# Kernel optimization log

Measured on AMD Instinct MI355X. Metric: run time of the kernel, lower is better.

Reference implementation:

```python
import jax, jax.numpy as jnp
import numpy as np

# Static config (matches init_kwargs)
DIM = 1024
INTER = 512
E = 8          # n_routed_experts
TOP_K = 2      # n_activated_experts
ROUTE_SCALE = 1.0


def setup_inputs() -> dict:
    key = jax.random.key(0)
    ks = jax.random.split(key, 8)
    s_d = 1.0 / np.sqrt(DIM)
    s_f = 1.0 / np.sqrt(INTER)
    x = jax.random.normal(ks[0], (2, 2048, DIM), dtype=jnp.float32)
    gate_w = jax.random.uniform(ks[1], (E, DIM), jnp.float32, -s_d, s_d)
    # routed expert weights, stacked: gate/up are [E, F, D], down is [E, D, F]
    wg = jax.random.uniform(ks[2], (E, INTER, DIM), jnp.float32, -s_d, s_d)
    wu = jax.random.uniform(ks[3], (E, INTER, DIM), jnp.float32, -s_d, s_d)
    wd = jax.random.uniform(ks[4], (E, DIM, INTER), jnp.float32, -s_f, s_f)
    # shared expert (n_shared_experts = 1)
    sg = jax.random.uniform(ks[5], (INTER, DIM), jnp.float32, -s_d, s_d)
    su = jax.random.uniform(ks[6], (INTER, DIM), jnp.float32, -s_d, s_d)
    sd = jax.random.uniform(ks[7], (DIM, INTER), jnp.float32, -s_f, s_f)
    return {"x": x, "gate_w": gate_w, "wg": wg, "wu": wu, "wd": wd,
            "sg": sg, "su": su, "sd": sd}


def reference(x, gate_w, wg, wu, wd, sg, su, sd):
    B, S, D = x.shape
    xf = x.reshape(-1, D)                       # [N, D]
    N = xf.shape[0]

    # ---- Gate (eval mode: no expert_bias, softmax scoring, 1 group) ----
    scores = jax.nn.softmax(xf @ gate_w.T, axis=-1)          # [N, E]
    _, idx = jax.lax.top_k(scores, TOP_K)                    # [N, K]
    weights = jnp.take_along_axis(scores, idx, axis=-1) * ROUTE_SCALE  # [N, K]

    # Combine weights as dense [N, E] (scatter-add of top-k weights) --
    # equivalent to the sort/dispatch + weighted scatter_add combine.
    cw = jnp.zeros((N, E), dtype=xf.dtype)
    cw = cw.at[jnp.arange(N)[:, None], idx].add(weights)     # [N, E]

    # ---- Routed experts: SwiGLU per expert ----
    g = jnp.einsum('nd,efd->nef', xf, wg)                    # [N, E, F]
    u = jnp.einsum('nd,efd->nef', xf, wu)                    # [N, E, F]
    h = jax.nn.silu(g) * u                                   # [N, E, F]
    y = jnp.einsum('nef,edf->ned', h, wd)                    # [N, E, D]
    routed = jnp.einsum('ned,ne->nd', y, cw)                 # [N, D]

    # ---- Shared expert (always active) ----
    shared = (jax.nn.silu(xf @ sg.T) * (xf @ su.T)) @ sd.T   # [N, D]

    return (routed + shared).reshape(B, S, D)
```

## Files before the change

kernel.cpp:

```cpp
#include <hip/hip_runtime.h>
#include <hip/hip_bf16.h>

constexpr int NTOK = 4096;
constexpr int DIMD = 1024;
constexpr int FINT = 512;
constexpr int NEXP = 8;

typedef __attribute__((ext_vector_type(8))) short bf16x8;
typedef __attribute__((ext_vector_type(4))) float f32x4;
typedef __attribute__((ext_vector_type(8))) unsigned short u16x8;

__device__ __forceinline__ f32x4 mfma16(bf16x8 a, bf16x8 b, f32x4 c) {
  return __builtin_amdgcn_mfma_f32_16x16x32_bf16(a, b, c, 0, 0, 0);
}

__device__ __forceinline__ void gload16(const void* g, void* l) {
  __builtin_amdgcn_global_load_lds(
      (const __attribute__((address_space(1))) void*)g,
      (__attribute__((address_space(3))) void*)l, 16, 0, 0);
}

__device__ __forceinline__ unsigned short f2bf(float f) {
  unsigned u = __float_as_uint(f);
  u += 0x7fffu + ((u >> 16) & 1u);
  return (unsigned short)(u >> 16);
}

__global__ __launch_bounds__(256) void cast_all(
    const float* __restrict__ x,  const float* __restrict__ wg,
    const float* __restrict__ wu, const float* __restrict__ wd,
    const float* __restrict__ sg, const float* __restrict__ su,
    const float* __restrict__ sd, const float* __restrict__ gw,
    unsigned short* __restrict__ xb,  unsigned short* __restrict__ w1b,
    unsigned short* __restrict__ wdb, unsigned short* __restrict__ s1b,
    unsigned short* __restrict__ sdb,
    int* __restrict__ eid, float2* __restrict__ w12) {
  const int seg = blockIdx.y;

  if (seg == 7) {
    if (blockIdx.x >= NTOK / 4) return;
    const int wid = threadIdx.x >> 6;
    const int lane = threadIdx.x & 63;
    const int n = blockIdx.x * 4 + wid;

    const float4* xr = (const float4*)(x + (size_t)n * DIMD);
    float4 xv[4];
#pragma unroll
    for (int j = 0; j < 4; ++j) xv[j] = xr[lane + 64 * j];

    double acc[NEXP];
#pragma unroll
    for (int e = 0; e < NEXP; ++e) {
      const float4* g = (const float4*)(gw + (size_t)e * DIMD);
      double a = 0.0;
#pragma unroll
      for (int j = 0; j < 4; ++j) {
        float4 gv = g[lane + 64 * j];
        a += (double)xv[j].x * (double)gv.x + (double)xv[j].y * (double)gv.y
           + (double)xv[j].z * (double)gv.z + (double)xv[j].w * (double)gv.w;
      }
      acc[e] = a;
    }
#pragma unroll
    for (int e = 0; e < NEXP; ++e) {
#pragma unroll
      for (int off = 32; off > 0; off >>= 1) acc[e] += __shfl_xor(acc[e], off);
    }

    if (lane == 0) {
      float logit[NEXP];
#pragma unroll
      for (int e = 0; e < NEXP; ++e) logit[e] = (float)acc[e];
      int i1 = 0; float v1 = logit[0];
#pragma unroll
      for (int e = 1; e < NEXP; ++e) if (logit[e] > v1) { v1 = logit[e]; i1 = e; }
      int i2 = -1; float v2 = -1e30f;
#pragma unroll
      for (int e = 0; e < NEXP; ++e) if (e != i1 && logit[e] > v2) { v2 = logit[e]; i2 = e; }
      float s = 0.f;
#pragma unroll
      for (int e = 0; e < NEXP; ++e) s += expf(logit[e] - v1);
      float w1 = 1.f / s;
      float w2 = expf(v2 - v1) / s;
      eid[n] = i1 | (i2 << 4);
      w12[n] = make_float2(w1, w2);
    }
    return;
  }

  const int i = blockIdx.x * 256 + threadIdx.x;
  const float* src; unsigned short* dst;
  size_t si = (size_t)i * 8, di;
  int n8;
  if (seg == 0) {
    n8 = NTOK * DIMD / 8; if (i >= n8) return;
    src = x; dst = xb; di = si;
  } else if (seg == 1 || seg == 2) {
    n8 = NEXP * FINT * DIMD / 8; if (i >= n8) return;
    int e = (int)(si >> 19), f = (int)((si >> 10) & 511), d = (int)(si & 1023);
    int r = ((f >> 4) << 5) + (seg == 2 ? 16 : 0) + (f & 15);
    src = (seg == 1) ? wg : wu; dst = w1b;
    di = (((size_t)e << 10) + r) * 1024 + d;
  } else if (seg == 3) {
    n8 = NEXP * DIMD * FINT / 8; if (i >= n8) return;
    src = wd; dst = wdb; di = si;
  } else if (seg == 4 || seg == 5) {
    n8 = FINT * DIMD / 8; if (i >= n8) return;
    int f = (int)((si >> 10) & 511), d = (int)(si & 1023);
    int r = ((f >> 4) << 5) + (seg == 5 ? 16 : 0) + (f & 15);
    src = (seg == 4) ? sg : su; dst = s1b;
    di = (size_t)r * 1024 + d;
  } else {
    n8 = DIMD * FINT / 8; if (i >= n8) return;
    src = sd; dst = sdb; di = si;
  }
  const float4* s4 = (const float4*)(src + si);
  float4 a = s4[0], b = s4[1];
  u16x8 o;
  o[0] = f2bf(a.x); o[1] = f2bf(a.y); o[2] = f2bf(a.z); o[3] = f2bf(a.w);
  o[4] = f2bf(b.x); o[5] = f2bf(b.y); o[6] = f2bf(b.z); o[7] = f2bf(b.w);
  *(u16x8*)(dst + di) = o;
}

__global__ __launch_bounds__(1024) void dispatch_scan(const int* __restrict__ eid,
                                                      const float2* __restrict__ w12,
                                                      int* __restrict__ cnt,
                                                      int* __restrict__ rowTok,
                                                      float* __restrict__ rowW,
                                                      int2* __restrict__ gslot) {
  const int th = threadIdx.x;
  const int lane = th & 63;
  const int wv = th >> 6;

  int e0[4], e1[4];
  float2 wp[4];
  unsigned long long c0 = 0, c1 = 0;
#pragma unroll
  for (int j = 0; j < 4; ++j) {
    int n = th * 4 + j;
    int p = eid[n];
    wp[j] = w12[n];
    int a = p & 15, b = (p >> 4) & 15;
    e0[j] = a; e1[j] = b;
    unsigned long long ia = 1ull << (16 * (a & 3));
    if (a < 4) c0 += ia; else c1 += ia;
    unsigned long long ib = 1ull << (16 * (b & 3));
    if (b < 4) c0 += ib; else c1 += ib;
  }

  unsigned long long s0 = c0, s1 = c1;
#pragma unroll
  for (int off = 1; off < 64; off <<= 1) {
    unsigned long long u0 = __shfl_up(s0, off);
    unsigned long long u1 = __shfl_up(s1, off);
    if (lane >= off) { s0 += u0; s1 += u1; }
  }

  __shared__ unsigned long long wt0[16], wt1[16];
  __shared__ int ebaseS[NEXP];
  if (lane == 63) { wt0[wv] = s0; wt1[wv] = s1; }
  __syncthreads();

  unsigned long long b0 = 0, b1 = 0;
  for (int w2 = 0; w2 < 16; ++w2)
    if (w2 < wv) { b0 += wt0[w2]; b1 += wt1[w2]; }

  if (th == 0) {
    unsigned long long t0 = 0, t1 = 0;
    for (int w2 = 0; w2 < 16; ++w2) { t0 += wt0[w2]; t1 += wt1[w2]; }
    int tot[NEXP];
#pragma unroll
    for (int e = 0; e < 4; ++e) {
      tot[e]     = (int)((t0 >> (16 * e)) & 0xffff);
      tot[e + 4] = (int)((t1 >> (16 * e)) & 0xffff);
    }
    int run = 0;
#pragma unroll
    for (int e = 0; e < NEXP; ++e) {
      cnt[e] = tot[e];
      cnt[8 + e] = run;
      ebaseS[e] = run;
      run += tot[e];
    }
  }

  unsigned long long x0 = b0 + s0 - c0;
  unsigned long long x1 = b1 + s1 - c1;

  __shared__ unsigned short posL[1024][8];
#pragma unroll
  for (int e = 0; e < 4; ++e) {
    posL[th][e]     = (unsigned short)((x0 >> (16 * e)) & 0xffff);
    posL[th][e + 4] = (unsigned short)((x1 >> (16 * e)) & 0xffff);
  }
  __syncthreads();

#pragma unroll
  for (int j = 0; j < 4; ++j) {
    int n = th * 4 + j;
    int a = e0[j];
    int pa = posL[th][a]; posL[th][a] = (unsigned short)(pa + 1);
    rowTok[a * NTOK + pa] = n; rowW[a * NTOK + pa] = wp[j].x;
    int b = e1[j];
    int pb = posL[th][b]; posL[th][b] = (unsigned short)(pb + 1);
    rowTok[b * NTOK + pb] = n; rowW[b * NTOK + pb] = wp[j].y;
    gslot[n] = make_int2(ebaseS[a] + pa, ebaseS[b] + pb);
  }
}


#define GEMM_TILE_LOOP(NT)                                                     \
  STAGE(0, 0, 0);                                                              \
  STAGE(0, 0, 1);                                                              \
  for (int tt = 0; tt < (NT); ++tt) {                                          \
    const int buf = tt & 1;                                                    \
    const unsigned char* LA0 = L + (buf * 2 + 0) * 16384;                      \
    const unsigned char* LB0 = LA0 + 65536;                                    \
    const unsigned char* LA1 = L + (buf * 2 + 1) * 16384;                      \
    const unsigned char* LB1 = LA1 + 65536;                                    \
    bf16x8 Af[4], Bf[4];                                                       \
                                                            \
    asm volatile("s_waitcnt vmcnt(4)" ::: "memory");                           \
    __builtin_amdgcn_sched_barrier(0);                                         \
    __builtin_amdgcn_s_barrier();                                              \
    __builtin_amdgcn_sched_barrier(0);                                         \
    _Pragma("unroll")                                                          \
    for (int n = 0; n < 4; ++n)                                                \
      Bf[n] = *(const bf16x8*)(LB0 + (wc * 64 + n * 16 + fr) * 64 + koffl);    \
    _Pragma("unroll")                                                          \
    for (int m = 0; m < 4; ++m)                                                \
      Af[m] = *(const bf16x8*)(LA0 + (wr * 128 + m * 16 + fr) * 64 + koffl);   \
    __builtin_amdgcn_s_setprio(1);                                             \
    _Pragma("unroll")                                                          \
    for (int n = 0; n < 4; ++n)                                                \
      _Pragma("unroll")                                                        \
      for (int m = 0; m < 4; ++m)                                              \
        acc[m][n] = mfma16(Af[m], Bf[n], acc[m][n]);                           \
    __builtin_amdgcn_s_setprio(0);                                             \
                                                            \
    if (tt + 1 < (NT)) STAGE(buf ^ 1, tt + 1, 0);                              \
    _Pragma("unroll")                                                          \
    for (int m = 0; m < 4; ++m)                                                \
      Af[m] = *(const bf16x8*)(LA0 + (wr * 128 + (m + 4) * 16 + fr) * 64 + koffl); \
    __builtin_amdgcn_s_setprio(1);                                             \
    _Pragma("unroll")                                                          \
    for (int n = 0; n < 4; ++n)                                                \
      _Pragma("unroll")                                                        \
      for (int m = 0; m < 4; ++m)                                              \
        acc[m + 4][n] = mfma16(Af[m], Bf[n], acc[m + 4][n]);                   \
    __builtin_amdgcn_s_setprio(0);                                             \
                                                            \
    if (tt + 1 < (NT)) asm volatile("s_waitcnt vmcnt(4)" ::: "memory");        \
    else               asm volatile("s_waitcnt vmcnt(0)" ::: "memory");        \
    __builtin_amdgcn_sched_barrier(0);                                         \
    __builtin_amdgcn_s_barrier();                                              \
    __builtin_amdgcn_sched_barrier(0);                                         \
    _Pragma("unroll")                                                          \
    for (int n = 0; n < 4; ++n)                                                \
      Bf[n] = *(const bf16x8*)(LB1 + (wc * 64 + n * 16 + fr) * 64 + koffl);    \
    _Pragma("unroll")                                                          \
    for (int m = 0; m < 4; ++m)                                                \
      Af[m] = *(const bf16x8*)(LA1 + (wr * 128 + m * 16 + fr) * 64 + koffl);   \
    __builtin_amdgcn_s_setprio(1);                                             \
    _Pragma("unroll")                                                          \
    for (int n = 0; n < 4; ++n)                                                \
      _Pragma("unroll")                                                        \
      for (int m = 0; m < 4; ++m)                                              \
        acc[m][n] = mfma16(Af[m], Bf[n], acc[m][n]);                           \
    __builtin_amdgcn_s_setprio(0);                                             \
                                                            \
    if (tt + 1 < (NT)) STAGE(buf ^ 1, tt + 1, 1);                              \
    _Pragma("unroll")                                                          \
    for (int m = 0; m < 4; ++m)                                                \
      Af[m] = *(const bf16x8*)(LA1 + (wr * 128 + (m + 4) * 16 + fr) * 64 + koffl); \
    __builtin_amdgcn_s_setprio(1);                                             \
    _Pragma("unroll")                                                          \
    for (int n = 0; n < 4; ++n)                                                \
      _Pragma("unroll")                                                        \
      for (int m = 0; m < 4; ++m)                                              \
        acc[m + 4][n] = mfma16(Af[m], Bf[n], acc[m + 4][n]);                   \
    __builtin_amdgcn_s_setprio(0);                                             \
  }

__global__ __launch_bounds__(512, 1) void gemm1_fused(
    const unsigned short* __restrict__ xb,
    const unsigned short* __restrict__ w1b,
    const unsigned short* __restrict__ s1b,
    unsigned short* __restrict__ hb,
    unsigned short* __restrict__ hs,
    const int* __restrict__ cnt,
    const int* __restrict__ rowTok,
    const unsigned short* __restrict__ zpg) {
  extern __shared__ unsigned char L[];
  const int e = blockIdx.x >> 2, ty = blockIdx.x & 3;
  const int tx = blockIdx.y;
  const bool RT = (e < NEXP);
  const int Te = RT ? cnt[e] : NTOK;
  const int m0 = tx * 256;
  if (m0 >= Te) return;
  const int n0 = ty * 256;

  const int t = threadIdx.x;
  const int w = t >> 6, lane = t & 63;
  const int wr = w >> 2, wc = w & 3;
  const int fr = lane & 15, hi = lane >> 4;
  const int koffl = ((hi ^ ((fr >> 1) & 3)) << 4);

  const unsigned short* w1e = RT ? w1b + (size_t)e * DIMD * DIMD : s1b;

  const unsigned short* apD[2];
  const unsigned short* bpD[2];
  int aoff[2], boff[2];
#pragma unroll
  for (int j = 0; j < 2; ++j) {
    int c = w * 128 + j * 64 + lane;
    int rowL = c >> 2;
    int seff = (c & 3) ^ ((c >> 3) & 3);
    int grow = m0 + rowL;
    const unsigned short* p;
    if (RT) p = (grow < Te) ? xb + (size_t)rowTok[e * NTOK + grow] * DIMD : zpg;
    else    p = xb + (size_t)grow * DIMD;
    apD[j] = p + seff * 8;
    bpD[j] = w1e + (size_t)(n0 + rowL) * DIMD + seff * 8;
    aoff[j] = c * 16;
    boff[j] = 65536 + c * 16;
  }

  f32x4 acc[8][4];
  f32x4 zero = {0.f, 0.f, 0.f, 0.f};
#pragma unroll
  for (int m = 0; m < 8; ++m)
#pragma unroll
    for (int n = 0; n < 4; ++n) acc[m][n] = zero;

  auto STAGE = [&](int buf, int tt, int q) {
    int slab = (buf * 2 + q) * 16384;
#pragma unroll
    for (int j = 0; j < 2; ++j) {
      gload16(apD[j] + tt * 64 + q * 32, L + slab + aoff[j]);
      gload16(bpD[j] + tt * 64 + q * 32, L + slab + boff[j]);
    }
  };

  GEMM_TILE_LOOP(DIMD / 64)

  unsigned short* hbase = RT ? hb + (size_t)cnt[8 + e] * FINT : hs;
  const int fbase = ty * 128 + wc * 32 + fr;
#pragma unroll
  for (int m = 0; m < 8; ++m) {
#pragma unroll
    for (int r = 0; r < 4; ++r) {
      int row = m0 + wr * 128 + m * 16 + hi * 4 + r;
      if (row < Te) {
        float g0 = acc[m][0][r], u0 = acc[m][1][r];
        float g1 = acc[m][2][r], u1 = acc[m][3][r];
        hbase[(size_t)row * FINT + fbase]      = f2bf(g0 / (1.f + expf(-g0)) * u0);
        hbase[(size_t)row * FINT + fbase + 16] = f2bf(g1 / (1.f + expf(-g1)) * u1);
      }
    }
  }
}

__global__ __launch_bounds__(512, 1) void gemm2_fused(
    const unsigned short* __restrict__ hb,
    const unsigned short* __restrict__ hs,
    const unsigned short* __restrict__ wdb,
    const unsigned short* __restrict__ sdb,
    float* __restrict__ ybuf,
    float* __restrict__ out,
    const int* __restrict__ cnt,
    const float* __restrict__ rowW,
    const unsigned short* __restrict__ zpg) {
  extern __shared__ unsigned char L[];
  const int e = blockIdx.x >> 2, ty = blockIdx.x & 3;
  const int tx = blockIdx.y;
  const bool RT = (e < NEXP);
  const int Te = RT ? cnt[e] : NTOK;
  const int m0 = tx * 256;
  if (m0 >= Te) return;
  const int n0 = ty * 256;

  const int t = threadIdx.x;
  const int w = t >> 6, lane = t & 63;
  const int wr = w >> 2, wc = w & 3;
  const int fr = lane & 15, hi = lane >> 4;
  const int koffl = ((hi ^ ((fr >> 1) & 3)) << 4);

  const int gbase = RT ? cnt[8 + e] : 0;
  const unsigned short* he  = RT ? hb + (size_t)gbase * FINT : hs;
  const unsigned short* wde = RT ? wdb + (size_t)e * DIMD * FINT : sdb;

  const unsigned short* apD[2];
  const unsigned short* bpD[2];
  int aoff[2], boff[2];
#pragma unroll
  for (int j = 0; j < 2; ++j) {
    int c = w * 128 + j * 64 + lane;
    int rowL = c >> 2;
    int seff = (c & 3) ^ ((c >> 3) & 3);
    int grow = m0 + rowL;
    apD[j] = ((grow < Te) ? he + (size_t)grow * FINT : zpg) + seff * 8;
    bpD[j] = wde + (size_t)(n0 + rowL) * FINT + seff * 8;
    aoff[j] = c * 16;
    boff[j] = 65536 + c * 16;
  }

  f32x4 acc[8][4];
  f32x4 zero = {0.f, 0.f, 0.f, 0.f};
#pragma unroll
  for (int m = 0; m < 8; ++m)
#pragma unroll
    for (int n = 0; n < 4; ++n) acc[m][n] = zero;

  auto STAGE = [&](int buf, int tt, int q) {
    int slab = (buf * 2 + q) * 16384;
#pragma unroll
    for (int j = 0; j < 2; ++j) {
      gload16(apD[j] + tt * 64 + q * 32, L + slab + aoff[j]);
      gload16(bpD[j] + tt * 64 + q * 32, L + slab + boff[j]);
    }
  };

  GEMM_TILE_LOOP(FINT / 64)

  const int colb = n0 + wc * 64;
#pragma unroll
  for (int m = 0; m < 8; ++m) {
#pragma unroll
    for (int r = 0; r < 4; ++r) {
      int row = m0 + wr * 128 + m * 16 + hi * 4 + r;
      if (row < Te) {
        if (RT) {
          float wt = rowW[e * NTOK + row];
          float* yr = ybuf + (size_t)(gbase + row) * DIMD;
#pragma unroll
          for (int n = 0; n < 4; ++n)
            yr[colb + n * 16 + fr] = wt * acc[m][n][r];
        } else {
          float* orow = out + (size_t)row * DIMD;
#pragma unroll
          for (int n = 0; n < 4; ++n)
            orow[colb + n * 16 + fr] = acc[m][n][r];
        }
      }
    }
  }
}

__global__ __launch_bounds__(256) void combine(const float* __restrict__ ybuf,
                                               const int2* __restrict__ gslot,
                                               float* __restrict__ out) {
  const int n = blockIdx.x;
  const int t = threadIdx.x;
  int2 gs = gslot[n];
  const float4* y1 = (const float4*)(ybuf + (size_t)gs.x * DIMD);
  const float4* y2 = (const float4*)(ybuf + (size_t)gs.y * DIMD);
  float4* o = (float4*)(out + (size_t)n * DIMD);
  float4 a = o[t], b = y1[t], c = y2[t];
  a.x += b.x + c.x; a.y += b.y + c.y; a.z += b.z + c.z; a.w += b.w + c.w;
  o[t] = a;
}

extern "C" void kernel_launch(void* const* d_in, const int* in_sizes, int n_in,
                              void* d_out, int out_size, void* d_ws, size_t ws_size,
                              hipStream_t stream) {
  const float* x  = (const float*)d_in[0];
  const float* gw = (const float*)d_in[1];
  const float* wg = (const float*)d_in[2];
  const float* wu = (const float*)d_in[3];
  const float* wd = (const float*)d_in[4];
  const float* sg = (const float*)d_in[5];
  const float* su = (const float*)d_in[6];
  const float* sd = (const float*)d_in[7];
  float* out = (float*)d_out;

  char* ws = (char*)d_ws;
  size_t off = 0;
  auto alloc = [&](size_t bytes) -> char* {
    char* p = ws + off;
    off += (bytes + 255) & ~(size_t)255;
    return p;
  };
  unsigned short* xb  = (unsigned short*)alloc((size_t)NTOK * DIMD * 2);
  unsigned short* w1b = (unsigned short*)alloc((size_t)NEXP * DIMD * DIMD * 2);
  unsigned short* wdb = (unsigned short*)alloc((size_t)NEXP * DIMD * FINT * 2);
  unsigned short* s1b = (unsigned short*)alloc((size_t)DIMD * DIMD * 2);
  unsigned short* sdb = (unsigned short*)alloc((size_t)DIMD * FINT * 2);
  unsigned short* hb  = (unsigned short*)alloc((size_t)2 * NTOK * FINT * 2);
  unsigned short* hs  = (unsigned short*)alloc((size_t)NTOK * FINT * 2);
  float*         ybuf = (float*)alloc((size_t)2 * NTOK * DIMD * 4);
  int*            cnt = (int*)alloc(256);
  int*         rowTok = (int*)alloc((size_t)NEXP * NTOK * 4);
  float*         rowW = (float*)alloc((size_t)NEXP * NTOK * 4);
  unsigned short* zpg = (unsigned short*)alloc((size_t)DIMD * 2);
  int*            eid = (int*)alloc((size_t)NTOK * 4);
  float2*         w12 = (float2*)alloc((size_t)NTOK * 8);
  int2*         gslot = (int2*)alloc((size_t)NTOK * 8);
  if (off > ws_size) return;

  hipFuncSetAttribute((const void*)gemm1_fused,
                      hipFuncAttributeMaxDynamicSharedMemorySize, 131072);
  hipFuncSetAttribute((const void*)gemm2_fused,
                      hipFuncAttributeMaxDynamicSharedMemorySize, 131072);

  hipMemsetAsync(zpg, 0, (size_t)DIMD * 2, stream);

  cast_all<<<dim3(2048, 8), 256, 0, stream>>>(x, wg, wu, wd, sg, su, sd, gw,
                                              xb, w1b, wdb, s1b, sdb, eid, w12);

  dispatch_scan<<<1, 1024, 0, stream>>>(eid, w12, cnt, rowTok, rowW, gslot);

  gemm1_fused<<<dim3(36, 16), 512, 131072, stream>>>(xb, w1b, s1b, hb, hs,
                                                     cnt, rowTok, zpg);
  gemm2_fused<<<dim3(36, 16), 512, 131072, stream>>>(hb, hs, wdb, sdb, ybuf, out,
                                                     cnt, rowW, zpg);
  combine<<<NTOK, 256, 0, stream>>>(ybuf, gslot, out);
}
```

Before: 111.9 us.

## Switch GEMMs to 32x32x16 MFMA and store routed outputs in bf16

Result: slower. 122.6 us (+9.5%).

```diff
diff --git a/kernel.cpp b/kernel.cpp
--- a/kernel.cpp
+++ b/kernel.cpp
@@ -7,11 +7,11 @@
 constexpr int NEXP = 8;
 
 typedef __attribute__((ext_vector_type(8))) short bf16x8;
-typedef __attribute__((ext_vector_type(4))) float f32x4;
+typedef __attribute__((ext_vector_type(16))) float f32x16;
 typedef __attribute__((ext_vector_type(8))) unsigned short u16x8;
 
-__device__ __forceinline__ f32x4 mfma16(bf16x8 a, bf16x8 b, f32x4 c) {
-  return __builtin_amdgcn_mfma_f32_16x16x32_bf16(a, b, c, 0, 0, 0);
+__device__ __forceinline__ f32x16 mfma32(bf16x8 a, bf16x8 b, f32x16 c) {
+  return __builtin_amdgcn_mfma_f32_32x32x16_bf16(a, b, c, 0, 0, 0);
 }
 
 __device__ __forceinline__ void gload16(const void* g, void* l) {
@@ -98,7 +98,7 @@
   } else if (seg == 1 || seg == 2) {
     n8 = NEXP * FINT * DIMD / 8; if (i >= n8) return;
     int e = (int)(si >> 19), f = (int)((si >> 10) & 511), d = (int)(si & 1023);
-    int r = ((f >> 4) << 5) + (seg == 2 ? 16 : 0) + (f & 15);
+    int r = ((f >> 5) << 6) + (f & 31) + (seg == 2 ? 32 : 0);
     src = (seg == 1) ? wg : wu; dst = w1b;
     di = (((size_t)e << 10) + r) * 1024 + d;
   } else if (seg == 3) {
@@ -107,7 +107,7 @@
   } else if (seg == 4 || seg == 5) {
     n8 = FINT * DIMD / 8; if (i >= n8) return;
     int f = (int)((si >> 10) & 511), d = (int)(si & 1023);
-    int r = ((f >> 4) << 5) + (seg == 5 ? 16 : 0) + (f & 15);
+    int r = ((f >> 5) << 6) + (f & 31) + (seg == 5 ? 32 : 0);
     src = (seg == 4) ? sg : su; dst = s1b;
     di = (size_t)r * 1024 + d;
   } else {
@@ -209,6 +209,21 @@
 }
 
 
+#define TILE_PHASE(LAx, LBx, KOFF)                                             \
+  _Pragma("unroll")                                                            \
+  for (int m = 0; m < 4; ++m)                                                  \
+    Af[m] = *(const bf16x8*)(LAx + (wr * 128 + m * 32 + l31) * 64 + (KOFF));   \
+  _Pragma("unroll")                                                            \
+  for (int n = 0; n < 2; ++n)                                                  \
+    Bf[n] = *(const bf16x8*)(LBx + (wc * 64 + n * 32 + l31) * 64 + (KOFF));    \
+  __builtin_amdgcn_s_setprio(1);                                               \
+  _Pragma("unroll")                                                            \
+  for (int n = 0; n < 2; ++n)                                                  \
+    _Pragma("unroll")                                                          \
+    for (int m = 0; m < 4; ++m)                                                \
+      acc[m][n] = mfma32(Af[m], Bf[n], acc[m][n]);                             \
+  __builtin_amdgcn_s_setprio(0);
+
 #define GEMM_TILE_LOOP(NT)                                                     \
   STAGE(0, 0, 0);                                                              \
   STAGE(0, 0, 1);                                                              \
@@ -218,68 +233,22 @@
     const unsigned char* LB0 = LA0 + 65536;                                    \
     const unsigned char* LA1 = L + (buf * 2 + 1) * 16384;                      \
     const unsigned char* LB1 = LA1 + 65536;                                    \
-    bf16x8 Af[4], Bf[4];                                                       \
-                                                            \
+    bf16x8 Af[4], Bf[2];                                                       \
     asm volatile("s_waitcnt vmcnt(4)" ::: "memory");                           \
     __builtin_amdgcn_sched_barrier(0);                                         \
     __builtin_amdgcn_s_barrier();                                              \
     __builtin_amdgcn_sched_barrier(0);                                         \
-    _Pragma("unroll")                                                          \
-    for (int n = 0; n < 4; ++n)                                                \
-      Bf[n] = *(const bf16x8*)(LB0 + (wc * 64 + n * 16 + fr) * 64 + koffl);    \
-    _Pragma("unroll")                                                          \
-    for (int m = 0; m < 4; ++m)                                                \
-      Af[m] = *(const bf16x8*)(LA0 + (wr * 128 + m * 16 + fr) * 64 + koffl);   \
-    __builtin_amdgcn_s_setprio(1);                                             \
-    _Pragma("unroll")                                                          \
-    for (int n = 0; n < 4; ++n)                                                \
-      _Pragma("unroll")                                                        \
-      for (int m = 0; m < 4; ++m)                                              \
-        acc[m][n] = mfma16(Af[m], Bf[n], acc[m][n]);                           \
-    __builtin_amdgcn_s_setprio(0);                                             \
-                                                            \
+    TILE_PHASE(LA0, LB0, koff0)                                                \
     if (tt + 1 < (NT)) STAGE(buf ^ 1, tt + 1, 0);                              \
-    _Pragma("unroll")                                                          \
-    for (int m = 0; m < 4; ++m)                                                \
-      Af[m] = *(const bf16x8*)(LA0 + (wr * 128 + (m + 4) * 16 + fr) * 64 + koffl); \
-    __builtin_amdgcn_s_setprio(1);                                             \
-    _Pragma("unroll")                                                          \
-    for (int n = 0; n < 4; ++n)                                                \
-      _Pragma("unroll")                                                        \
-      for (int m = 0; m < 4; ++m)                                              \
-        acc[m + 4][n] = mfma16(Af[m], Bf[n], acc[m + 4][n]);                   \
-    __builtin_amdgcn_s_setprio(0);                                             \
-                                                            \
+    TILE_PHASE(LA0, LB0, koff1)                                                \
     if (tt + 1 < (NT)) asm volatile("s_waitcnt vmcnt(4)" ::: "memory");        \
     else               asm volatile("s_waitcnt vmcnt(0)" ::: "memory");        \
     __builtin_amdgcn_sched_barrier(0);                                         \
     __builtin_amdgcn_s_barrier();                                              \
     __builtin_amdgcn_sched_barrier(0);                                         \
-    _Pragma("unroll")                                                          \
-    for (int n = 0; n < 4; ++n)                                                \
-      Bf[n] = *(const bf16x8*)(LB1 + (wc * 64 + n * 16 + fr) * 64 + koffl);    \
-    _Pragma("unroll")                                                          \
-    for (int m = 0; m < 4; ++m)                                                \
-      Af[m] = *(const bf16x8*)(LA1 + (wr * 128 + m * 16 + fr) * 64 + koffl);   \
-    __builtin_amdgcn_s_setprio(1);                                             \
-    _Pragma("unroll")                                                          \
-    for (int n = 0; n < 4; ++n)                                                \
-      _Pragma("unroll")                                                        \
-      for (int m = 0; m < 4; ++m)                                              \
-        acc[m][n] = mfma16(Af[m], Bf[n], acc[m][n]);                           \
-    __builtin_amdgcn_s_setprio(0);                                             \
-                                                            \
+    TILE_PHASE(LA1, LB1, koff0)                                                \
     if (tt + 1 < (NT)) STAGE(buf ^ 1, tt + 1, 1);                              \
-    _Pragma("unroll")                                                          \
-    for (int m = 0; m < 4; ++m)                                                \
-      Af[m] = *(const bf16x8*)(LA1 + (wr * 128 + (m + 4) * 16 + fr) * 64 + koffl); \
-    __builtin_amdgcn_s_setprio(1);                                             \
-    _Pragma("unroll")                                                          \
-    for (int n = 0; n < 4; ++n)                                                \
-      _Pragma("unroll")                                                        \
-      for (int m = 0; m < 4; ++m)                                              \
-        acc[m + 4][n] = mfma16(Af[m], Bf[n], acc[m + 4][n]);                   \
-    __builtin_amdgcn_s_setprio(0);                                             \
+    TILE_PHASE(LA1, LB1, koff1)                                                \
   }
 
 __global__ __launch_bounds__(512, 1) void gemm1_fused(
@@ -303,8 +272,10 @@
   const int t = threadIdx.x;
   const int w = t >> 6, lane = t & 63;
   const int wr = w >> 2, wc = w & 3;
-  const int fr = lane & 15, hi = lane >> 4;
-  const int koffl = ((hi ^ ((fr >> 1) & 3)) << 4);
+  const int l31 = lane & 31, l5 = lane >> 5;
+  const int sb = (l31 >> 1) & 3;
+  const int koff0 = ((l5) ^ sb) * 16;
+  const int koff1 = ((2 | l5) ^ sb) * 16;
 
   const unsigned short* w1e = RT ? w1b + (size_t)e * DIMD * DIMD : s1b;
 
@@ -326,12 +297,13 @@
     boff[j] = 65536 + c * 16;
   }
 
-  f32x4 acc[8][4];
-  f32x4 zero = {0.f, 0.f, 0.f, 0.f};
-#pragma unroll
-  for (int m = 0; m < 8; ++m)
-#pragma unroll
-    for (int n = 0; n < 4; ++n) acc[m][n] = zero;
+  f32x16 acc[4][2];
+#pragma unroll
+  for (int m = 0; m < 4; ++m)
+#pragma unroll
+    for (int n = 0; n < 2; ++n)
+#pragma unroll
+      for (int r = 0; r < 16; ++r) acc[m][n][r] = 0.f;
 
   auto STAGE = [&](int buf, int tt, int q) {
     int slab = (buf * 2 + q) * 16384;
@@ -345,17 +317,15 @@
   GEMM_TILE_LOOP(DIMD / 64)
 
   unsigned short* hbase = RT ? hb + (size_t)cnt[8 + e] * FINT : hs;
-  const int fbase = ty * 128 + wc * 32 + fr;
-#pragma unroll
-  for (int m = 0; m < 8; ++m) {
-#pragma unroll
-    for (int r = 0; r < 4; ++r) {
-      int row = m0 + wr * 128 + m * 16 + hi * 4 + r;
+  const int fcol = ((ty * 4 + wc) << 5) + l31;
+#pragma unroll
+  for (int m = 0; m < 4; ++m) {
+#pragma unroll
+    for (int r = 0; r < 16; ++r) {
+      int row = m0 + wr * 128 + m * 32 + (r & 3) + 8 * (r >> 2) + 4 * l5;
       if (row < Te) {
-        float g0 = acc[m][0][r], u0 = acc[m][1][r];
-        float g1 = acc[m][2][r], u1 = acc[m][3][r];
-        hbase[(size_t)row * FINT + fbase]      = f2bf(g0 / (1.f + expf(-g0)) * u0);
-        hbase[(size_t)row * FINT + fbase + 16] = f2bf(g1 / (1.f + expf(-g1)) * u1);
+        float g = acc[m][0][r], u = acc[m][1][r];
+        hbase[(size_t)row * FINT + fcol] = f2bf(g / (1.f + expf(-g)) * u);
       }
     }
   }
@@ -366,7 +336,7 @@
     const unsigned short* __restrict__ hs,
     const unsigned short* __restrict__ wdb,
     const unsigned short* __restrict__ sdb,
-    float* __restrict__ ybuf,
+    unsigned short* __restrict__ ybuf,
     float* __restrict__ out,
     const int* __restrict__ cnt,
     const float* __restrict__ rowW,
@@ -383,8 +353,10 @@
   const int t = threadIdx.x;
   const int w = t >> 6, lane = t & 63;
   const int wr = w >> 2, wc = w & 3;
-  const int fr = lane & 15, hi = lane >> 4;
-  const int koffl = ((hi ^ ((fr >> 1) & 3)) << 4);
+  const int l31 = lane & 31, l5 = lane >> 5;
+  const int sb = (l31 >> 1) & 3;
+  const int koff0 = ((l5) ^ sb) * 16;
+  const int koff1 = ((2 | l5) ^ sb) * 16;
 
   const int gbase = RT ? cnt[8 + e] : 0;
   const unsigned short* he  = RT ? hb + (size_t)gbase * FINT : hs;
@@ -405,12 +377,13 @@
     boff[j] = 65536 + c * 16;
   }
 
-  f32x4 acc[8][4];
-  f32x4 zero = {0.f, 0.f, 0.f, 0.f};
-#pragma unroll
-  for (int m = 0; m < 8; ++m)
-#pragma unroll
-    for (int n = 0; n < 4; ++n) acc[m][n] = zero;
+  f32x16 acc[4][2];
+#pragma unroll
+  for (int m = 0; m < 4; ++m)
+#pragma unroll
+    for (int n = 0; n < 2; ++n)
+#pragma unroll
+      for (int r = 0; r < 16; ++r) acc[m][n][r] = 0.f;
 
   auto STAGE = [&](int buf, int tt, int q) {
     int slab = (buf * 2 + q) * 16384;
@@ -423,42 +396,43 @@
 
   GEMM_TILE_LOOP(FINT / 64)
 
-  const int colb = n0 + wc * 64;
-#pragma unroll
-  for (int m = 0; m < 8; ++m) {
-#pragma unroll
-    for (int r = 0; r < 4; ++r) {
-      int row = m0 + wr * 128 + m * 16 + hi * 4 + r;
+  const int colb = n0 + wc * 64 + l31;
+#pragma unroll
+  for (int m = 0; m < 4; ++m) {
+#pragma unroll
+    for (int r = 0; r < 16; ++r) {
+      int row = m0 + wr * 128 + m * 32 + (r & 3) + 8 * (r >> 2) + 4 * l5;
       if (row < Te) {
         if (RT) {
           float wt = rowW[e * NTOK + row];
-          float* yr = ybuf + (size_t)(gbase + row) * DIMD;
-#pragma unroll
-          for (int n = 0; n < 4; ++n)
-            yr[colb + n * 16 + fr] = wt * acc[m][n][r];
+          unsigned short* yr = ybuf + (size_t)(gbase + row) * DIMD;
+          yr[colb]      = f2bf(wt * acc[m][0][r]);
+          yr[colb + 32] = f2bf(wt * acc[m][1][r]);
         } else {
           float* orow = out + (size_t)row * DIMD;
-#pragma unroll
-          for (int n = 0; n < 4; ++n)
-            orow[colb + n * 16 + fr] = acc[m][n][r];
+          orow[colb]      = acc[m][0][r];
+          orow[colb + 32] = acc[m][1][r];
         }
       }
     }
   }
 }
 
-__global__ __launch_bounds__(256) void combine(const float* __restrict__ ybuf,
+__global__ __launch_bounds__(256) void combine(const unsigned short* __restrict__ ybuf,
                                                const int2* __restrict__ gslot,
                                                float* __restrict__ out) {
   const int n = blockIdx.x;
   const int t = threadIdx.x;
   int2 gs = gslot[n];
-  const float4* y1 = (const float4*)(ybuf + (size_t)gs.x * DIMD);
-  const float4* y2 = (const float4*)(ybuf + (size_t)gs.y * DIMD);
-  float4* o = (float4*)(out + (size_t)n * DIMD);
-  float4 a = o[t], b = y1[t], c = y2[t];
-  a.x += b.x + c.x; a.y += b.y + c.y; a.z += b.z + c.z; a.w += b.w + c.w;
-  o[t] = a;
+  ushort4 a = ((const ushort4*)(ybuf + (size_t)gs.x * DIMD))[t];
+  ushort4 b = ((const ushort4*)(ybuf + (size_t)gs.y * DIMD))[t];
+  float4* op = (float4*)(out + (size_t)n * DIMD);
+  float4 o = op[t];
+  o.x += __uint_as_float((unsigned)a.x << 16) + __uint_as_float((unsigned)b.x << 16);
+  o.y += __uint_as_float((unsigned)a.y << 16) + __uint_as_float((unsigned)b.y << 16);
+  o.z += __uint_as_float((unsigned)a.z << 16) + __uint_as_float((unsigned)b.z << 16);
+  o.w += __uint_as_float((unsigned)a.w << 16) + __uint_as_float((unsigned)b.w << 16);
+  op[t] = o;
 }
 
 extern "C" void kernel_launch(void* const* d_in, const int* in_sizes, int n_in,
@@ -488,7 +462,7 @@
   unsigned short* sdb = (unsigned short*)alloc((size_t)DIMD * FINT * 2);
   unsigned short* hb  = (unsigned short*)alloc((size_t)2 * NTOK * FINT * 2);
   unsigned short* hs  = (unsigned short*)alloc((size_t)NTOK * FINT * 2);
-  float*         ybuf = (float*)alloc((size_t)2 * NTOK * DIMD * 4);
+  unsigned short* ybuf= (unsigned short*)alloc((size_t)2 * NTOK * DIMD * 2);
   int*            cnt = (int*)alloc(256);
   int*         rowTok = (int*)alloc((size_t)NEXP * NTOK * 4);
   float*         rowW = (float*)alloc((size_t)NEXP * NTOK * 4);
```

## Fold dispatch scan into cast kernel, stage epilogues through LDS, store bf16 expert outputs

Applied to the files above, without the earlier changes.

Measured after the change: 169.7 us. 1.52x slower.

```diff
diff --git a/kernel.cpp b/kernel.cpp
--- a/kernel.cpp
+++ b/kernel.cpp
@@ -24,6 +24,10 @@
   unsigned u = __float_as_uint(f);
   u += 0x7fffu + ((u >> 16) & 1u);
   return (unsigned short)(u >> 16);
+}
+
+__device__ __forceinline__ float bf2f(unsigned short v) {
+  return __uint_as_float((unsigned)v << 16);
 }
 
 __global__ __launch_bounds__(256) void cast_all(
@@ -34,7 +38,10 @@
     unsigned short* __restrict__ xb,  unsigned short* __restrict__ w1b,
     unsigned short* __restrict__ wdb, unsigned short* __restrict__ s1b,
     unsigned short* __restrict__ sdb,
-    int* __restrict__ eid, float2* __restrict__ w12) {
+    int* __restrict__ eid, float2* __restrict__ w12,
+    int* __restrict__ done,
+    int* __restrict__ cnt, int* __restrict__ rowTok,
+    float* __restrict__ rowW, int2* __restrict__ gslot) {
   const int seg = blockIdx.y;
 
   if (seg == 7) {
@@ -43,47 +50,130 @@
     const int lane = threadIdx.x & 63;
     const int n = blockIdx.x * 4 + wid;
 
-    const float4* xr = (const float4*)(x + (size_t)n * DIMD);
-    float4 xv[4];
-#pragma unroll
-    for (int j = 0; j < 4; ++j) xv[j] = xr[lane + 64 * j];
-
-    double acc[NEXP];
-#pragma unroll
-    for (int e = 0; e < NEXP; ++e) {
-      const float4* g = (const float4*)(gw + (size_t)e * DIMD);
-      double a = 0.0;
-#pragma unroll
-      for (int j = 0; j < 4; ++j) {
-        float4 gv = g[lane + 64 * j];
-        a += (double)xv[j].x * (double)gv.x + (double)xv[j].y * (double)gv.y
-           + (double)xv[j].z * (double)gv.z + (double)xv[j].w * (double)gv.w;
+    {
+      const float4* xr = (const float4*)(x + (size_t)n * DIMD);
+      float4 xv[4];
+#pragma unroll
+      for (int j = 0; j < 4; ++j) xv[j] = xr[lane + 64 * j];
+
+      double acc[NEXP];
+#pragma unroll
+      for (int e = 0; e < NEXP; ++e) {
+        const float4* g = (const float4*)(gw + (size_t)e * DIMD);
+        double a = 0.0;
+#pragma unroll
+        for (int j = 0; j < 4; ++j) {
+          float4 gv = g[lane + 64 * j];
+          a += (double)xv[j].x * (double)gv.x + (double)xv[j].y * (double)gv.y
+             + (double)xv[j].z * (double)gv.z + (double)xv[j].w * (double)gv.w;
+        }
+        acc[e] = a;
       }
-      acc[e] = a;
-    }
-#pragma unroll
-    for (int e = 0; e < NEXP; ++e) {
-#pragma unroll
-      for (int off = 32; off > 0; off >>= 1) acc[e] += __shfl_xor(acc[e], off);
-    }
-
-    if (lane == 0) {
-      float logit[NEXP];
-#pragma unroll
-      for (int e = 0; e < NEXP; ++e) logit[e] = (float)acc[e];
-      int i1 = 0; float v1 = logit[0];
-#pragma unroll
-      for (int e = 1; e < NEXP; ++e) if (logit[e] > v1) { v1 = logit[e]; i1 = e; }
-      int i2 = -1; float v2 = -1e30f;
-#pragma unroll
-      for (int e = 0; e < NEXP; ++e) if (e != i1 && logit[e] > v2) { v2 = logit[e]; i2 = e; }
-      float s = 0.f;
-#pragma unroll
-      for (int e = 0; e < NEXP; ++e) s += expf(logit[e] - v1);
-      float w1 = 1.f / s;
-      float w2 = expf(v2 - v1) / s;
-      eid[n] = i1 | (i2 << 4);
-      w12[n] = make_float2(w1, w2);
+#pragma unroll
+      for (int e = 0; e < NEXP; ++e) {
+#pragma unroll
+        for (int off = 32; off > 0; off >>= 1) acc[e] += __shfl_xor(acc[e], off);
+      }
+
+      if (lane == 0) {
+        float logit[NEXP];
+#pragma unroll
+        for (int e = 0; e < NEXP; ++e) logit[e] = (float)acc[e];
+        int i1 = 0; float v1 = logit[0];
+#pragma unroll
+        for (int e = 1; e < NEXP; ++e) if (logit[e] > v1) { v1 = logit[e]; i1 = e; }
+        int i2 = -1; float v2 = -1e30f;
+#pragma unroll
+        for (int e = 0; e < NEXP; ++e) if (e != i1 && logit[e] > v2) { v2 = logit[e]; i2 = e; }
+        float s = 0.f;
+#pragma unroll
+        for (int e = 0; e < NEXP; ++e) s += expf(logit[e] - v1);
+        eid[n] = i1 | (i2 << 4);
+        w12[n] = make_float2(1.f / s, expf(v2 - v1) / s);
+      }
+    }
+
+    __shared__ int lastFlag;
+    __threadfence();
+    __syncthreads();
+    if (threadIdx.x == 0) {
+      int old = atomicAdd(done, 1);
+      lastFlag = (old == NTOK / 4 - 1) ? 1 : 0;
+    }
+    __syncthreads();
+    if (!lastFlag) return;
+    __threadfence();
+
+    const int th = threadIdx.x;
+    const int ln = th & 63;
+    const int wv = th >> 6;
+
+    int ea[16], eb[16];
+    float2 wp[16];
+    unsigned long long c0 = 0, c1 = 0;
+#pragma unroll
+    for (int j = 0; j < 16; ++j) {
+      int n2 = th * 16 + j;
+      int p = eid[n2];
+      wp[j] = w12[n2];
+      int a = p & 15, b = (p >> 4) & 15;
+      ea[j] = a; eb[j] = b;
+      unsigned long long ia = 1ull << (16 * (a & 3));
+      if (a < 4) c0 += ia; else c1 += ia;
+      unsigned long long ib = 1ull << (16 * (b & 3));
+      if (b < 4) c0 += ib; else c1 += ib;
+    }
+    unsigned long long s0 = c0, s1 = c1;
+#pragma unroll
+    for (int off = 1; off < 64; off <<= 1) {
+      unsigned long long u0 = __shfl_up(s0, off);
+      unsigned long long u1 = __shfl_up(s1, off);
+      if (ln >= off) { s0 += u0; s1 += u1; }
+    }
+    __shared__ unsigned long long wt0S[4], wt1S[4];
+    __shared__ int ebaseS[NEXP];
+    __shared__ unsigned short posL[256][8];
+    if (ln == 63) { wt0S[wv] = s0; wt1S[wv] = s1; }
+    __syncthreads();
+    unsigned long long b0 = 0, b1 = 0;
+    for (int w2 = 0; w2 < 4; ++w2)
+      if (w2 < wv) { b0 += wt0S[w2]; b1 += wt1S[w2]; }
+    if (th == 0) {
+      unsigned long long t0 = 0, t1 = 0;
+      for (int w2 = 0; w2 < 4; ++w2) { t0 += wt0S[w2]; t1 += wt1S[w2]; }
+      int tot[NEXP];
+#pragma unroll
+      for (int e = 0; e < 4; ++e) {
+        tot[e]     = (int)((t0 >> (16 * e)) & 0xffff);
+        tot[e + 4] = (int)((t1 >> (16 * e)) & 0xffff);
+      }
+      int run = 0;
+#pragma unroll
+      for (int e = 0; e < NEXP; ++e) {
+        cnt[e] = tot[e];
+        cnt[8 + e] = run;
+        ebaseS[e] = run;
+        run += tot[e];
+      }
+    }
+    unsigned long long x0 = b0 + s0 - c0;
+    unsigned long long x1 = b1 + s1 - c1;
+#pragma unroll
+    for (int e = 0; e < 4; ++e) {
+      posL[th][e]     = (unsigned short)((x0 >> (16 * e)) & 0xffff);
+      posL[th][e + 4] = (unsigned short)((x1 >> (16 * e)) & 0xffff);
+    }
+    __syncthreads();
+#pragma unroll
+    for (int j = 0; j < 16; ++j) {
+      int n2 = th * 16 + j;
+      int a = ea[j];
+      int pa = posL[th][a]; posL[th][a] = (unsigned short)(pa + 1);
+      rowTok[a * NTOK + pa] = n2; rowW[a * NTOK + pa] = wp[j].x;
+      int b = eb[j];
+      int pb = posL[th][b]; posL[th][b] = (unsigned short)(pb + 1);
+      rowTok[b * NTOK + pb] = n2; rowW[b * NTOK + pb] = wp[j].y;
+      gslot[n2] = make_int2(ebaseS[a] + pa, ebaseS[b] + pb);
     }
     return;
   }
@@ -122,92 +212,6 @@
   *(u16x8*)(dst + di) = o;
 }
 
-__global__ __launch_bounds__(1024) void dispatch_scan(const int* __restrict__ eid,
-                                                      const float2* __restrict__ w12,
-                                                      int* __restrict__ cnt,
-                                                      int* __restrict__ rowTok,
-                                                      float* __restrict__ rowW,
-                                                      int2* __restrict__ gslot) {
-  const int th = threadIdx.x;
-  const int lane = th & 63;
-  const int wv = th >> 6;
-
-  int e0[4], e1[4];
-  float2 wp[4];
-  unsigned long long c0 = 0, c1 = 0;
-#pragma unroll
-  for (int j = 0; j < 4; ++j) {
-    int n = th * 4 + j;
-    int p = eid[n];
-    wp[j] = w12[n];
-    int a = p & 15, b = (p >> 4) & 15;
-    e0[j] = a; e1[j] = b;
-    unsigned long long ia = 1ull << (16 * (a & 3));
-    if (a < 4) c0 += ia; else c1 += ia;
-    unsigned long long ib = 1ull << (16 * (b & 3));
-    if (b < 4) c0 += ib; else c1 += ib;
-  }
-
-  unsigned long long s0 = c0, s1 = c1;
-#pragma unroll
-  for (int off = 1; off < 64; off <<= 1) {
-    unsigned long long u0 = __shfl_up(s0, off);
-    unsigned long long u1 = __shfl_up(s1, off);
-    if (lane >= off) { s0 += u0; s1 += u1; }
-  }
-
-  __shared__ unsigned long long wt0[16], wt1[16];
-  __shared__ int ebaseS[NEXP];
-  if (lane == 63) { wt0[wv] = s0; wt1[wv] = s1; }
-  __syncthreads();
-
-  unsigned long long b0 = 0, b1 = 0;
-  for (int w2 = 0; w2 < 16; ++w2)
-    if (w2 < wv) { b0 += wt0[w2]; b1 += wt1[w2]; }
-
-  if (th == 0) {
-    unsigned long long t0 = 0, t1 = 0;
-    for (int w2 = 0; w2 < 16; ++w2) { t0 += wt0[w2]; t1 += wt1[w2]; }
-    int tot[NEXP];
-#pragma unroll
-    for (int e = 0; e < 4; ++e) {
-      tot[e]     = (int)((t0 >> (16 * e)) & 0xffff);
-      tot[e + 4] = (int)((t1 >> (16 * e)) & 0xffff);
-    }
-    int run = 0;
-#pragma unroll
-    for (int e = 0; e < NEXP; ++e) {
-      cnt[e] = tot[e];
-      cnt[8 + e] = run;
-      ebaseS[e] = run;
-      run += tot[e];
-    }
-  }
-
-  unsigned long long x0 = b0 + s0 - c0;
-  unsigned long long x1 = b1 + s1 - c1;
-
-  __shared__ unsigned short posL[1024][8];
-#pragma unroll
-  for (int e = 0; e < 4; ++e) {
-    posL[th][e]     = (unsigned short)((x0 >> (16 * e)) & 0xffff);
-    posL[th][e + 4] = (unsigned short)((x1 >> (16 * e)) & 0xffff);
-  }
-  __syncthreads();
-
-#pragma unroll
-  for (int j = 0; j < 4; ++j) {
-    int n = th * 4 + j;
-    int a = e0[j];
-    int pa = posL[th][a]; posL[th][a] = (unsigned short)(pa + 1);
-    rowTok[a * NTOK + pa] = n; rowW[a * NTOK + pa] = wp[j].x;
-    int b = e1[j];
-    int pb = posL[th][b]; posL[th][b] = (unsigned short)(pb + 1);
-    rowTok[b * NTOK + pb] = n; rowW[b * NTOK + pb] = wp[j].y;
-    gslot[n] = make_int2(ebaseS[a] + pa, ebaseS[b] + pb);
-  }
-}
-
 
 #define GEMM_TILE_LOOP(NT)                                                     \
   STAGE(0, 0, 0);                                                              \
@@ -344,20 +348,29 @@
 
   GEMM_TILE_LOOP(DIMD / 64)
 
+  __syncthreads();
+  unsigned short* HL = (unsigned short*)L;
+#pragma unroll
+  for (int m = 0; m < 8; ++m) {
+#pragma unroll
+    for (int r = 0; r < 4; ++r) {
+      int rl = wr * 128 + m * 16 + hi * 4 + r;
+      float g0 = acc[m][0][r], u0 = acc[m][1][r];
+      float g1 = acc[m][2][r], u1 = acc[m][3][r];
+      HL[rl * 128 + wc * 32 + fr]      = f2bf(g0 / (1.f + expf(-g0)) * u0);
+      HL[rl * 128 + wc * 32 + 16 + fr] = f2bf(g1 / (1.f + expf(-g1)) * u1);
+    }
+  }
+  __syncthreads();
   unsigned short* hbase = RT ? hb + (size_t)cnt[8 + e] * FINT : hs;
-  const int fbase = ty * 128 + wc * 32 + fr;
-#pragma unroll
-  for (int m = 0; m < 8; ++m) {
-#pragma unroll
-    for (int r = 0; r < 4; ++r) {
-      int row = m0 + wr * 128 + m * 16 + hi * 4 + r;
-      if (row < Te) {
-        float g0 = acc[m][0][r], u0 = acc[m][1][r];
-        float g1 = acc[m][2][r], u1 = acc[m][3][r];
-        hbase[(size_t)row * FINT + fbase]      = f2bf(g0 / (1.f + expf(-g0)) * u0);
-        hbase[(size_t)row * FINT + fbase + 16] = f2bf(g1 / (1.f + expf(-g1)) * u1);
-      }
-    }
+  const int f0 = n0 >> 1;
+#pragma unroll
+  for (int it = 0; it < 8; ++it) {
+    int cid = it * 512 + t;
+    int row = cid >> 4, c8 = cid & 15;
+    if (m0 + row < Te)
+      *(u16x8*)(hbase + (size_t)(m0 + row) * FINT + f0 + c8 * 8) =
+          *(const u16x8*)(HL + row * 128 + c8 * 8);
   }
 }
 
@@ -366,8 +379,8 @@
     const unsigned short* __restrict__ hs,
     const unsigned short* __restrict__ wdb,
     const unsigned short* __restrict__ sdb,
-    float* __restrict__ ybuf,
-    float* __restrict__ out,
+    unsigned short* __restrict__ ybuf,
+    unsigned short* __restrict__ ys,
     const int* __restrict__ cnt,
     const float* __restrict__ rowW,
     const unsigned short* __restrict__ zpg) {
@@ -423,42 +436,47 @@
 
   GEMM_TILE_LOOP(FINT / 64)
 
-  const int colb = n0 + wc * 64;
+  __syncthreads();
+  unsigned short* YL = (unsigned short*)L;
 #pragma unroll
   for (int m = 0; m < 8; ++m) {
 #pragma unroll
     for (int r = 0; r < 4; ++r) {
-      int row = m0 + wr * 128 + m * 16 + hi * 4 + r;
-      if (row < Te) {
-        if (RT) {
-          float wt = rowW[e * NTOK + row];
-          float* yr = ybuf + (size_t)(gbase + row) * DIMD;
-#pragma unroll
-          for (int n = 0; n < 4; ++n)
-            yr[colb + n * 16 + fr] = wt * acc[m][n][r];
-        } else {
-          float* orow = out + (size_t)row * DIMD;
-#pragma unroll
-          for (int n = 0; n < 4; ++n)
-            orow[colb + n * 16 + fr] = acc[m][n][r];
-        }
-      }
-    }
-  }
-}
-
-__global__ __launch_bounds__(256) void combine(const float* __restrict__ ybuf,
+      int rl = wr * 128 + m * 16 + hi * 4 + r;
+      float wt = RT ? rowW[e * NTOK + m0 + rl] : 1.f;
+#pragma unroll
+      for (int n = 0; n < 4; ++n)
+        YL[rl * 256 + wc * 64 + n * 16 + fr] = f2bf(wt * acc[m][n][r]);
+    }
+  }
+  __syncthreads();
+  unsigned short* ybase = RT ? ybuf + (size_t)gbase * DIMD : ys;
+#pragma unroll
+  for (int it = 0; it < 16; ++it) {
+    int cid = it * 512 + t;
+    int row = cid >> 5, c8 = cid & 31;
+    if (m0 + row < Te)
+      *(u16x8*)(ybase + (size_t)(m0 + row) * DIMD + n0 + c8 * 8) =
+          *(const u16x8*)(YL + row * 256 + c8 * 8);
+  }
+}
+
+__global__ __launch_bounds__(256) void combine(const unsigned short* __restrict__ ybuf,
+                                               const unsigned short* __restrict__ ys,
                                                const int2* __restrict__ gslot,
                                                float* __restrict__ out) {
   const int n = blockIdx.x;
   const int t = threadIdx.x;
   int2 gs = gslot[n];
-  const float4* y1 = (const float4*)(ybuf + (size_t)gs.x * DIMD);
-  const float4* y2 = (const float4*)(ybuf + (size_t)gs.y * DIMD);
-  float4* o = (float4*)(out + (size_t)n * DIMD);
-  float4 a = o[t], b = y1[t], c = y2[t];
-  a.x += b.x + c.x; a.y += b.y + c.y; a.z += b.z + c.z; a.w += b.w + c.w;
-  o[t] = a;
+  ushort4 a = ((const ushort4*)(ybuf + (size_t)gs.x * DIMD))[t];
+  ushort4 b = ((const ushort4*)(ybuf + (size_t)gs.y * DIMD))[t];
+  ushort4 c = ((const ushort4*)(ys + (size_t)n * DIMD))[t];
+  float4 o;
+  o.x = bf2f(c.x) + bf2f(a.x) + bf2f(b.x);
+  o.y = bf2f(c.y) + bf2f(a.y) + bf2f(b.y);
+  o.z = bf2f(c.z) + bf2f(a.z) + bf2f(b.z);
+  o.w = bf2f(c.w) + bf2f(a.w) + bf2f(b.w);
+  ((float4*)(out + (size_t)n * DIMD))[t] = o;
 }
 
 extern "C" void kernel_launch(void* const* d_in, const int* in_sizes, int n_in,
@@ -488,7 +506,8 @@
   unsigned short* sdb = (unsigned short*)alloc((size_t)DIMD * FINT * 2);
   unsigned short* hb  = (unsigned short*)alloc((size_t)2 * NTOK * FINT * 2);
   unsigned short* hs  = (unsigned short*)alloc((size_t)NTOK * FINT * 2);
-  float*         ybuf = (float*)alloc((size_t)2 * NTOK * DIMD * 4);
+  unsigned short* ybuf= (unsigned short*)alloc((size_t)2 * NTOK * DIMD * 2);
+  unsigned short* ys  = (unsigned short*)alloc((size_t)NTOK * DIMD * 2);
   int*            cnt = (int*)alloc(256);
   int*         rowTok = (int*)alloc((size_t)NEXP * NTOK * 4);
   float*         rowW = (float*)alloc((size_t)NEXP * NTOK * 4);
@@ -496,6 +515,7 @@
   int*            eid = (int*)alloc((size_t)NTOK * 4);
   float2*         w12 = (float2*)alloc((size_t)NTOK * 8);
   int2*         gslot = (int2*)alloc((size_t)NTOK * 8);
+  int*           done = (int*)alloc(256);
   if (off > ws_size) return;
 
   hipFuncSetAttribute((const void*)gemm1_fused,
@@ -504,15 +524,15 @@
                       hipFuncAttributeMaxDynamicSharedMemorySize, 131072);
 
   hipMemsetAsync(zpg, 0, (size_t)DIMD * 2, stream);
+  hipMemsetAsync(done, 0, 256, stream);
 
   cast_all<<<dim3(2048, 8), 256, 0, stream>>>(x, wg, wu, wd, sg, su, sd, gw,
-                                              xb, w1b, wdb, s1b, sdb, eid, w12);
-
-  dispatch_scan<<<1, 1024, 0, stream>>>(eid, w12, cnt, rowTok, rowW, gslot);
+                                              xb, w1b, wdb, s1b, sdb, eid, w12,
+                                              done, cnt, rowTok, rowW, gslot);
 
   gemm1_fused<<<dim3(36, 16), 512, 131072, stream>>>(xb, w1b, s1b, hb, hs,
                                                      cnt, rowTok, zpg);
-  gemm2_fused<<<dim3(36, 16), 512, 131072, stream>>>(hb, hs, wdb, sdb, ybuf, out,
+  gemm2_fused<<<dim3(36, 16), 512, 131072, stream>>>(hb, hs, wdb, sdb, ybuf, ys,
                                                      cnt, rowW, zpg);
-  combine<<<NTOK, 256, 0, stream>>>(ybuf, gslot, out);
-}
+  combine<<<NTOK, 256, 0, stream>>>(ybuf, ys, gslot, out);
+}
```
